# Optimization experiments

Hardware: AMD Instinct MI355X
Metric: run time of the kernel (lower is better)

Reference implementation:

```python
import jax, jax.numpy as jnp
import numpy as np

SOS = 1
V, H, B, T = 32000, 1024, 32, 64


def setup_inputs() -> dict:
    key = jax.random.key(0)
    ks = jax.random.split(key, 9)
    scale = 1.0 / np.sqrt(H)
    return {
        "encoder_outputs": jax.random.normal(ks[0], (B, T, H), dtype=jnp.float32),
        "encoder_hidden": jax.random.normal(ks[1], (1, B, H), dtype=jnp.float32),
        "target_tensor": jax.random.randint(ks[2], (B, T), 0, V),
        "embedding": jax.random.normal(ks[3], (V, H), dtype=jnp.float32),
        "w_ih": jax.random.uniform(ks[4], (3 * H, H), jnp.float32, -scale, scale),
        "w_hh": jax.random.uniform(ks[5], (3 * H, H), jnp.float32, -scale, scale),
        "b_ih": jax.random.uniform(ks[6], (3 * H,), jnp.float32, -scale, scale),
        "b_hh": jax.random.uniform(ks[7], (3 * H,), jnp.float32, -scale, scale),
        "w_out": jax.random.uniform(ks[8], (V, H), jnp.float32, -scale, scale),
        "b_out": jnp.zeros((V,), dtype=jnp.float32),
    }


def _gru_cell(x, h, w_ih, w_hh, b_ih, b_hh):
    # PyTorch GRU cell: gates ordered (r, z, n)
    gi = x @ w_ih.T + b_ih            # [B, 3H]
    gh = h @ w_hh.T + b_hh            # [B, 3H]
    i_r, i_z, i_n = jnp.split(gi, 3, axis=-1)
    h_r, h_z, h_n = jnp.split(gh, 3, axis=-1)
    r = jax.nn.sigmoid(i_r + h_r)
    z = jax.nn.sigmoid(i_z + h_z)
    n = jnp.tanh(i_n + r * h_n)
    return (1.0 - z) * n + z * h


def reference(encoder_outputs, encoder_hidden, target_tensor, embedding,
              w_ih, w_hh, b_ih, b_hh, w_out, b_out):
    batch = encoder_outputs.shape[0]
    # teacher-forced input tokens: [SOS, y_0, ..., y_{T-2}] -> [T, B]
    sos = jnp.full((batch, 1), SOS, dtype=target_tensor.dtype)
    tokens = jnp.concatenate([sos, target_tensor[:, :-1]], axis=1).T  # [T, B]

    h0 = encoder_hidden[0]  # [B, H]

    def step(h, tok):
        x = jax.nn.relu(embedding[tok])            # [B, H]
        h_new = _gru_cell(x, h, w_ih, w_hh, b_ih, b_hh)
        return h_new, h_new

    h_last, hs = jax.lax.scan(step, h0, tokens)    # hs: [T, B, H]
    logits = jnp.einsum('tbh,vh->btv', hs, w_out) + b_out  # [B, T, V]
    log_probs = jax.nn.log_softmax(logits, axis=-1)
    return log_probs, h_last[None]  # hidden returned as [1, B, H]
```

## Files before the change

### kernel.cpp

```cpp
#include <hip/hip_runtime.h>
#include <stdint.h>

#define Hd 1024
#define Bd 32
#define Td 64
#define Vd 32000
#define TB (Td*Bd)
#define G3H 3072
#define NB 64
#define JC 16
static const size_t BTV = (size_t)Bd * Td * Vd;

typedef unsigned short u16;
typedef __attribute__((ext_vector_type(8))) short bf16x8;
typedef __attribute__((ext_vector_type(4))) float f32x4;
typedef __attribute__((ext_vector_type(4))) unsigned int u32x4;

typedef __attribute__((address_space(3))) void lds_void;
typedef __attribute__((address_space(1))) const void gbl_void;

__device__ __forceinline__ void async_ld16(const void* g, void* l) {
    __builtin_amdgcn_global_load_lds((gbl_void*)g, (lds_void*)l, 16, 0, 0);
}

__device__ __forceinline__ u16 f2bf(float f) {
    union { float f; uint32_t u; } v; v.f = f;
    uint32_t u = v.u;
    return (u16)((u + 0x7fffu + ((u >> 16) & 1u)) >> 16);
}

__device__ __forceinline__ u32x4 gload_b128_sc(const u16* p) {
    u32x4 r;
    asm volatile("global_load_dwordx4 %0, %1, off sc0 sc1"
                 : "=v"(r) : "v"(p) : "memory");
    return r;
}
__device__ __forceinline__ void gstore_b32_sc(u16* p, unsigned int v) {
    asm volatile("global_store_dword %0, %1, off sc0 sc1"
                 :: "v"(p), "v"(v) : "memory");
}

__device__ __forceinline__ float fsigmoid(float x) {
    return __builtin_amdgcn_rcpf(1.f + __expf(-x));
}
__device__ __forceinline__ float ftanh(float x) {
    return 1.f - 2.f * __builtin_amdgcn_rcpf(1.f + __expf(2.f * x));
}

__global__ void k_conv_bf16(const float* __restrict__ src, u16* __restrict__ dst, int n4) {
    int i = blockIdx.x * blockDim.x + threadIdx.x;
    if (i >= n4) return;
    float4 f = ((const float4*)src)[i];
    ushort4 o;
    o.x = f2bf(f.x); o.y = f2bf(f.y); o.z = f2bf(f.z); o.w = f2bf(f.w);
    ((ushort4*)dst)[i] = o;
}

__global__ void k_embed(const float* __restrict__ emb, const int* __restrict__ tgt,
                        u16* __restrict__ Xb) {
    int r = blockIdx.x;
    int t = r >> 5, b = r & 31;
    int tok = (t == 0) ? 1 : tgt[b * Td + (t - 1)];
    const float4* srow = (const float4*)(emb + (size_t)tok * Hd);
    int k = threadIdx.x;
    float4 f = srow[k];
    ushort4 o;
    o.x = f2bf(fmaxf(f.x, 0.f)); o.y = f2bf(fmaxf(f.y, 0.f));
    o.z = f2bf(fmaxf(f.z, 0.f)); o.w = f2bf(fmaxf(f.w, 0.f));
    ((ushort4*)(Xb + (size_t)r * Hd))[k] = o;
}

__global__ void k_init_h(const float* __restrict__ eh, u16* __restrict__ hb,
                         unsigned int* __restrict__ cnt) {
    if (blockIdx.x == 0 && threadIdx.x == 0) *cnt = 0u;
    int i = blockIdx.x * blockDim.x + threadIdx.x;
    float4 f = ((const float4*)eh)[i];
    ushort4 o;
    o.x = f2bf(f.x); o.y = f2bf(f.y); o.z = f2bf(f.z); o.w = f2bf(f.w);
    ((ushort4*)hb)[i] = o;
}

template<int MODE, int SWAP>
__global__ __launch_bounds__(256, 2)
void k_gemm128(const u16* __restrict__ A, const u16* __restrict__ Bm,
               const float* __restrict__ bias, float* __restrict__ C,
               int N, int K)
{
    __shared__ alignas(16) u16 As[128 * 32];
    __shared__ alignas(16) u16 Bs[128 * 32];
    const int tid  = threadIdx.x;
    const int wave = tid >> 6;
    const int lane = tid & 63;
    const int l16  = lane & 15;
    const int q    = lane >> 4;
    const int wm   = (wave & 1) << 6;
    const int wn   = (wave >> 1) << 6;
    const int tm   = (SWAP ? blockIdx.x : blockIdx.y) << 7;
    const int tn   = (SWAP ? blockIdx.y : blockIdx.x) << 7;

    f32x4 acc[4][4];
#pragma unroll
    for (int i = 0; i < 4; ++i)
#pragma unroll
        for (int j = 0; j < 4; ++j) { f32x4 z = {0.f,0.f,0.f,0.f}; acc[i][j] = z; }

    const int c0 = wave * 2, c1 = wave * 2 + 1;
    const int cr = lane >> 2;
    const int kg = lane & 3;
    const u16* gA0 = A + (size_t)(tm + c0*16 + cr) * K + kg*8;
    const u16* gA1 = A + (size_t)(tm + c1*16 + cr) * K + kg*8;
    const u16* gB0 = Bm + (size_t)(tn + c0*16 + cr) * K + kg*8;
    const u16* gB1 = Bm + (size_t)(tn + c1*16 + cr) * K + kg*8;
    u16* lA0 = &As[c0*512 + lane*8];
    u16* lA1 = &As[c1*512 + lane*8];
    u16* lB0 = &Bs[c0*512 + lane*8];
    u16* lB1 = &Bs[c1*512 + lane*8];

    for (int k0 = 0; k0 < K; k0 += 32) {
        async_ld16(gA0 + k0, lA0);
        async_ld16(gA1 + k0, lA1);
        async_ld16(gB0 + k0, lB0);
        async_ld16(gB1 + k0, lB1);
        __syncthreads();
        bf16x8 af[4], bfr[4];
#pragma unroll
        for (int i = 0; i < 4; ++i)
            af[i] = *(const bf16x8*)&As[(wm + i*16 + l16) * 32 + q*8];
#pragma unroll
        for (int j = 0; j < 4; ++j)
            bfr[j] = *(const bf16x8*)&Bs[(wn + j*16 + l16) * 32 + q*8];
#pragma unroll
        for (int i = 0; i < 4; ++i)
#pragma unroll
            for (int j = 0; j < 4; ++j)
                acc[i][j] = __builtin_amdgcn_mfma_f32_16x16x32_bf16(af[i], bfr[j], acc[i][j], 0, 0, 0);
        __syncthreads();
    }

#pragma unroll
    for (int i = 0; i < 4; ++i) {
        const int mbase = tm + wm + i*16 + q*4;
#pragma unroll
        for (int j = 0; j < 4; ++j) {
            const int n = tn + wn + j*16 + l16;
            const float bv = bias[n];
#pragma unroll
            for (int r = 0; r < 4; ++r) {
                const int m = mbase + r;
                const float v = acc[i][j][r] + bv;
                if (MODE == 0) {
                    C[(size_t)m * N + n] = v;
                } else {
                    const int tt = m >> 5, bb = m & 31;
                    C[(size_t)((bb << 6) + tt) * Vd + n] = v;
                }
            }
        }
    }
}

__global__ __launch_bounds__(256, 1)
void k_gru_persist(const float* __restrict__ gi,
                   const float* __restrict__ enc_h,
                   const u16* __restrict__ w_hhb,
                   const float* __restrict__ b_hh,
                   u16* __restrict__ hbA, u16* __restrict__ hbB,
                   u16* __restrict__ hsb, float* __restrict__ hlast,
                   unsigned int* __restrict__ cnt)
{
    __shared__ alignas(16) u16 Ws[48 * 1024];
    __shared__ float ghs[2][3][32][17];
    const int tid = threadIdx.x;
    const int j0  = blockIdx.x * JC;

    for (int idx = tid; idx < 48 * 128; idx += 256) {
        int gr = idx >> 7;
        int c  = idx & 127;
        const u16* src = w_hhb + (size_t)((gr >> 4) * Hd + j0 + (gr & 15)) * Hd + c * 8;
        *(bf16x8*)&Ws[(size_t)(c * 48 + gr) * 8] = *(const bf16x8*)src;
    }

    const int b  = tid >> 3;
    const int jp = (tid & 7) * 2;
    float h0 = enc_h[b * Hd + j0 + jp];
    float h1 = enc_h[b * Hd + j0 + jp + 1];
    const float br0 = b_hh[j0 + jp],           br1 = b_hh[j0 + jp + 1];
    const float bz0 = b_hh[Hd + j0 + jp],      bz1 = b_hh[Hd + j0 + jp + 1];
    const float bn0 = b_hh[2*Hd + j0 + jp],    bn1 = b_hh[2*Hd + j0 + jp + 1];

    const int wave = tid >> 6, lane = tid & 63;
    const int l16 = lane & 15, q = lane >> 4;
    const int mh = wave & 1, kh = wave >> 1;

    __syncthreads();

    for (int t = 0; t < Td; ++t) {
        const u16* hb_in  = (t & 1) ? hbB : hbA;
        u16*       hb_out = (t & 1) ? hbA : hbB;
        const int row = t * 32 + b;
        const float* gir = gi + (size_t)row * G3H;

        const u16* ap = hb_in + (size_t)(mh*16 + l16) * Hd + kh*512 + q*8;
        u32x4 areg[16];
#pragma unroll
        for (int it = 0; it < 16; ++it)
            areg[it] = gload_b128_sc(ap + it*32);

        const float gr0 = gir[j0 + jp],          gr1 = gir[j0 + jp + 1];
        const float gz0 = gir[Hd + j0 + jp],     gz1 = gir[Hd + j0 + jp + 1];
        const float gn0 = gir[2*Hd + j0 + jp],   gn1 = gir[2*Hd + j0 + jp + 1];

        asm volatile("s_waitcnt vmcnt(0)" ::: "memory");

        f32x4 acc0 = {0.f,0.f,0.f,0.f}, acc1 = acc0, acc2 = acc0;
#pragma unroll
        for (int it = 0; it < 16; ++it) {
            bf16x8 a = __builtin_bit_cast(bf16x8, areg[it]);
            const int kgrp = kh*64 + it*4 + q;
            const u16* wp = &Ws[(size_t)(kgrp * 48 + l16) * 8];
            bf16x8 w0 = *(const bf16x8*)(wp);
            bf16x8 w1 = *(const bf16x8*)(wp + 16*8);
            bf16x8 w2 = *(const bf16x8*)(wp + 32*8);
            acc0 = __builtin_amdgcn_mfma_f32_16x16x32_bf16(a, w0, acc0, 0, 0, 0);
            acc1 = __builtin_amdgcn_mfma_f32_16x16x32_bf16(a, w1, acc1, 0, 0, 0);
            acc2 = __builtin_amdgcn_mfma_f32_16x16x32_bf16(a, w2, acc2, 0, 0, 0);
        }
#pragma unroll
        for (int r = 0; r < 4; ++r) {
            const int bb = mh*16 + q*4 + r;
            ghs[kh][0][bb][l16] = acc0[r];
            ghs[kh][1][bb][l16] = acc1[r];
            ghs[kh][2][bb][l16] = acc2[r];
        }
        __syncthreads();

        {
            const float hr0 = ghs[0][0][b][jp]   + ghs[1][0][b][jp]   + br0;
            const float hr1 = ghs[0][0][b][jp+1] + ghs[1][0][b][jp+1] + br1;
            const float hz0 = ghs[0][1][b][jp]   + ghs[1][1][b][jp]   + bz0;
            const float hz1 = ghs[0][1][b][jp+1] + ghs[1][1][b][jp+1] + bz1;
            const float hn0 = ghs[0][2][b][jp]   + ghs[1][2][b][jp]   + bn0;
            const float hn1 = ghs[0][2][b][jp+1] + ghs[1][2][b][jp+1] + bn1;
            const float rg0 = fsigmoid(gr0 + hr0);
            const float rg1 = fsigmoid(gr1 + hr1);
            const float zg0 = fsigmoid(gz0 + hz0);
            const float zg1 = fsigmoid(gz1 + hz1);
            const float ng0 = ftanh(gn0 + rg0 * hn0);
            const float ng1 = ftanh(gn1 + rg1 * hn1);
            h0 = (1.f - zg0) * ng0 + zg0 * h0;
            h1 = (1.f - zg1) * ng1 + zg1 * h1;
            ushort2 pv; pv.x = f2bf(h0); pv.y = f2bf(h1);
            const unsigned int pw = (unsigned int)pv.x | ((unsigned int)pv.y << 16);
            gstore_b32_sc(&hb_out[b * Hd + j0 + jp], pw);
            *(ushort2*)&hsb[(size_t)row * Hd + j0 + jp] = pv;
            if (t == Td - 1) {
                hlast[b * Hd + j0 + jp]     = h0;
                hlast[b * Hd + j0 + jp + 1] = h1;
            }
        }

        if (t < Td - 1) {
            __syncthreads();
            if (tid == 0) atomicAdd(cnt, 1u);
            const unsigned tgt = (unsigned)(t + 1) * NB;
            while (__hip_atomic_load(cnt, __ATOMIC_RELAXED, __HIP_MEMORY_SCOPE_AGENT) < tgt)
                __builtin_amdgcn_s_sleep(1);
        }
    }
}

__global__ __launch_bounds__(256)
void k_logsoftmax(float* __restrict__ out) {
    float* row = out + (size_t)blockIdx.x * Vd;
    const int tid = threadIdx.x;
    float m = -1e30f, s = 0.f;
    for (int i = tid * 4; i + 3 < Vd; i += 1024) {
        float4 f = *(const float4*)(row + i);
        float lm = fmaxf(fmaxf(f.x, f.y), fmaxf(f.z, f.w));
        if (lm > m) { s *= __expf(m - lm); m = lm; }
        s += __expf(f.x - m) + __expf(f.y - m) + __expf(f.z - m) + __expf(f.w - m);
    }
    for (int off = 32; off > 0; off >>= 1) {
        float mo = __shfl_down(m, off, 64);
        float so = __shfl_down(s, off, 64);
        float M = fmaxf(m, mo);
        s = s * __expf(m - M) + so * __expf(mo - M);
        m = M;
    }
    __shared__ float sm[4], ss[4];
    const int wave = tid >> 6, lane = tid & 63;
    if (lane == 0) { sm[wave] = m; ss[wave] = s; }
    __syncthreads();
    const float M = fmaxf(fmaxf(sm[0], sm[1]), fmaxf(sm[2], sm[3]));
    const float S = ss[0]*__expf(sm[0]-M) + ss[1]*__expf(sm[1]-M)
                  + ss[2]*__expf(sm[2]-M) + ss[3]*__expf(sm[3]-M);
    const float lz = M + logf(S);
    for (int i = tid * 4; i + 3 < Vd; i += 1024) {
        float4 f = *(const float4*)(row + i);
        f.x -= lz; f.y -= lz; f.z -= lz; f.w -= lz;
        *(float4*)(row + i) = f;
    }
}

extern "C" void kernel_launch(void* const* d_in, const int* in_sizes, int n_in,
                              void* d_out, int out_size, void* d_ws, size_t ws_size,
                              hipStream_t stream) {
    const float* enc_h = (const float*)d_in[1];
    const int*   tgt   = (const int*)d_in[2];
    const float* emb   = (const float*)d_in[3];
    const float* w_ih  = (const float*)d_in[4];
    const float* w_hh  = (const float*)d_in[5];
    const float* b_ih  = (const float*)d_in[6];
    const float* b_hh  = (const float*)d_in[7];
    const float* w_out = (const float*)d_in[8];
    const float* b_out = (const float*)d_in[9];
    float* out = (float*)d_out;

    char* ws = (char*)d_ws;
    size_t off = 0;
    auto alloc = [&](size_t bytes) { void* p = ws + off; off += (bytes + 255) & ~(size_t)255; return p; };
    u16*   w_outb = (u16*)  alloc((size_t)Vd * Hd * 2);
    u16*   w_ihb  = (u16*)  alloc((size_t)G3H * Hd * 2);
    u16*   w_hhb  = (u16*)  alloc((size_t)G3H * Hd * 2);
    u16*   Xb     = (u16*)  alloc((size_t)TB * Hd * 2);
    u16*   hsb    = (u16*)  alloc((size_t)TB * Hd * 2);
    float* gi     = (float*)alloc((size_t)TB * G3H * 4);
    u16*   hb0    = (u16*)  alloc((size_t)Bd * Hd * 2);
    u16*   hb1    = (u16*)  alloc((size_t)Bd * Hd * 2);
    unsigned int* cnt = (unsigned int*) alloc(256);
    (void)ws_size; (void)in_sizes; (void)n_in; (void)out_size;

    k_conv_bf16<<<(Vd*Hd/4 + 255)/256, 256, 0, stream>>>(w_out, w_outb, Vd*Hd/4);
    k_conv_bf16<<<(G3H*Hd/4 + 255)/256, 256, 0, stream>>>(w_ih, w_ihb, G3H*Hd/4);
    k_conv_bf16<<<(G3H*Hd/4 + 255)/256, 256, 0, stream>>>(w_hh, w_hhb, G3H*Hd/4);
    k_embed<<<TB, 256, 0, stream>>>(emb, tgt, Xb);
    k_init_h<<<32, 256, 0, stream>>>(enc_h, hb0, cnt);

    k_gemm128<0,0><<<dim3(G3H/128, TB/128), 256, 0, stream>>>(Xb, w_ihb, b_ih, gi, G3H, Hd);

    k_gru_persist<<<NB, 256, 0, stream>>>(gi, enc_h, w_hhb, b_hh, hb0, hb1, hsb,
                                          out + BTV, cnt);

    k_gemm128<1,1><<<dim3(TB/128, Vd/128), 256, 0, stream>>>(hsb, w_outb, b_out, out, Vd, Hd);

    k_logsoftmax<<<TB, 256, 0, stream>>>(out);
}
```

Before: 1.085 ms.

## Replace atomic counter grid barrier with per-block flags and prefetch next gate inputs

Swaps the single shared atomic counter used as the per-timestep grid barrier in the persistent GRU kernel for one flag per block. Each block stores its step number with a cache-bypassing store, and wave 0 polls all 64 flags at once with a wave-wide all-reduce before a block barrier. The input-gate values for the next step are loaded during the barrier wait, taking them off the critical path. This is meant to remove atomic contention and serialisation on one address, at the cost of 64 polled loads per spin and an extra __syncthreads per step. It relies on the counter buffer holding at least NB entries.

```diff
diff --git a/kernel.cpp b/kernel.cpp
--- a/kernel.cpp
+++ b/kernel.cpp
@@ -36,6 +36,10 @@
     return r;
 }
 __device__ __forceinline__ void gstore_b32_sc(u16* p, unsigned int v) {
+    asm volatile("global_store_dword %0, %1, off sc0 sc1"
+                 :: "v"(p), "v"(v) : "memory");
+}
+__device__ __forceinline__ void gstore_u32_sc(unsigned int* p, unsigned int v) {
     asm volatile("global_store_dword %0, %1, off sc0 sc1"
                  :: "v"(p), "v"(v) : "memory");
 }
@@ -72,7 +76,7 @@
 
 __global__ void k_init_h(const float* __restrict__ eh, u16* __restrict__ hb,
                          unsigned int* __restrict__ cnt) {
-    if (blockIdx.x == 0 && threadIdx.x == 0) *cnt = 0u;
+    if (blockIdx.x == 0 && threadIdx.x < NB) cnt[threadIdx.x] = 0u;
     int i = blockIdx.x * blockDim.x + threadIdx.x;
     float4 f = ((const float4*)eh)[i];
     ushort4 o;
@@ -192,23 +196,26 @@
     const int l16 = lane & 15, q = lane >> 4;
     const int mh = wave & 1, kh = wave >> 1;
 
+    float gr0, gr1, gz0, gz1, gn0, gn1;
+    {
+        const float* gir = gi + (size_t)b * G3H;
+        gr0 = gir[j0 + jp];        gr1 = gir[j0 + jp + 1];
+        gz0 = gir[Hd + j0 + jp];   gz1 = gir[Hd + j0 + jp + 1];
+        gn0 = gir[2*Hd + j0 + jp]; gn1 = gir[2*Hd + j0 + jp + 1];
+    }
+
     __syncthreads();
 
     for (int t = 0; t < Td; ++t) {
         const u16* hb_in  = (t & 1) ? hbB : hbA;
         u16*       hb_out = (t & 1) ? hbA : hbB;
         const int row = t * 32 + b;
-        const float* gir = gi + (size_t)row * G3H;
 
         const u16* ap = hb_in + (size_t)(mh*16 + l16) * Hd + kh*512 + q*8;
         u32x4 areg[16];
 #pragma unroll
         for (int it = 0; it < 16; ++it)
             areg[it] = gload_b128_sc(ap + it*32);
-
-        const float gr0 = gir[j0 + jp],          gr1 = gir[j0 + jp + 1];
-        const float gz0 = gir[Hd + j0 + jp],     gz1 = gir[Hd + j0 + jp + 1];
-        const float gn0 = gir[2*Hd + j0 + jp],   gn1 = gir[2*Hd + j0 + jp + 1];
 
         asm volatile("s_waitcnt vmcnt(0)" ::: "memory");
 
@@ -261,10 +268,21 @@
 
         if (t < Td - 1) {
             __syncthreads();
-            if (tid == 0) atomicAdd(cnt, 1u);
-            const unsigned tgt = (unsigned)(t + 1) * NB;
-            while (__hip_atomic_load(cnt, __ATOMIC_RELAXED, __HIP_MEMORY_SCOPE_AGENT) < tgt)
-                __builtin_amdgcn_s_sleep(1);
+            if (tid == 0)
+                gstore_u32_sc(&cnt[blockIdx.x], (unsigned)(t + 1));
+            {
+                const float* gir = gi + (size_t)((t + 1) * 32 + b) * G3H;
+                gr0 = gir[j0 + jp];        gr1 = gir[j0 + jp + 1];
+                gz0 = gir[Hd + j0 + jp];   gz1 = gir[Hd + j0 + jp + 1];
+                gn0 = gir[2*Hd + j0 + jp]; gn1 = gir[2*Hd + j0 + jp + 1];
+            }
+            if (wave == 0) {
+                const unsigned tgt = (unsigned)(t + 1);
+                while (!__all(__hip_atomic_load(&cnt[lane], __ATOMIC_RELAXED,
+                                                __HIP_MEMORY_SCOPE_AGENT) >= tgt))
+                    __builtin_amdgcn_s_sleep(2);
+            }
+            __syncthreads();
         }
     }
 }
```

Result: no change. 1.094 ms (+0.8%).
